# Optimization experiments

Measured on AMD Instinct MI355X. Metric: run time of the kernel, lower is better.

Reference implementation:

```python
import jax, jax.numpy as jnp
import numpy as np

B, D_IN, D, D_OUT, N_BLOCKS = 32768, 100, 1024, 1, 5
H = 0.1
EPS = 1e-4


def setup_inputs() -> dict:
    key = jax.random.key(0)
    ks = jax.random.split(key, 10)
    x = jax.random.normal(ks[0], (B, D_IN), dtype=jnp.float32)
    # first linear: D_IN -> D
    W0 = jax.random.normal(ks[1], (D, D_IN), dtype=jnp.float32) / np.sqrt(D_IN)
    b0 = jnp.zeros((D,), dtype=jnp.float32)
    # middle residual linears: D -> D, stacked over blocks
    Ws = jax.random.normal(ks[2], (N_BLOCKS, D, D), dtype=jnp.float32) / np.sqrt(D)
    bs = jnp.zeros((N_BLOCKS, D), dtype=jnp.float32)
    # brownian Linear(D, 1, bias=False) weight vectors, one per block
    bw = jax.random.normal(ks[3], (N_BLOCKS, D), dtype=jnp.float32) / np.sqrt(D)
    # last linear: D -> D_OUT
    Wlast = jax.random.normal(ks[4], (D_OUT, D), dtype=jnp.float32) / np.sqrt(D)
    blast = jnp.zeros((D_OUT,), dtype=jnp.float32)
    # torch.rand_like(out): uniform [0,1) noise per block
    noise = jax.random.uniform(ks[5], (N_BLOCKS, B, D), dtype=jnp.float32)
    return {"x": x, "W0": W0, "b0": b0, "Ws": Ws, "bs": bs,
            "bw": bw, "Wlast": Wlast, "blast": blast, "noise": noise}


def reference(x, W0, b0, Ws, bs, bw, Wlast, blast, noise):
    sqrt_h = H ** 0.5
    out = jnp.tanh(x @ W0.T + b0)  # [B, D]
    for i in range(N_BLOCKS):
        z = noise[i]  # [B, D]
        w = bw[i]     # [D]
        # product(): z @ (w w^T + eps I)^T = (z.w) w + eps z  (rank-1, O(D))
        proj = (z @ w)[:, None] * w + EPS * z
        out = out + H * jnp.tanh(out @ Ws[i].T + bs[i]) + sqrt_h * proj
    return out @ Wlast.T + blast  # [B, D_OUT]
```

## Files before the change

### kernel.cpp

```cpp
#include <hip/hip_runtime.h>
#include <hip/hip_bf16.h>


typedef unsigned short u16;
typedef __attribute__((ext_vector_type(8))) short short8;
typedef __attribute__((ext_vector_type(8))) u16 u16x8;
typedef __attribute__((ext_vector_type(4))) u16 u16x4;
typedef __attribute__((ext_vector_type(4))) float f32x4;
typedef __attribute__((ext_vector_type(16))) float f32x16;

#define BROWS 32768
#define DDIM 1024
#define NBLK 5
#define H_STEP 0.1f
#define SQRT_H 0.31622776601683794f

#define FENCE() asm volatile("" ::: "memory")
#define BARRIER() do { FENCE(); __builtin_amdgcn_s_barrier(); FENCE(); } while (0)

__device__ __forceinline__ float bf2f(u16 u) {
    return __uint_as_float(((unsigned)u) << 16);
}
__device__ __forceinline__ u16 f2bf(float f) {
    unsigned u = __float_as_uint(f);
    unsigned r = 0x7fffu + ((u >> 16) & 1u);
    return (u16)((u + r) >> 16);
}
__device__ __forceinline__ float fast_tanh(float s) {
    float e = __expf(2.0f * s);
    return 1.0f - 2.0f * __builtin_amdgcn_rcpf(e + 1.0f);
}

#define GLOAD_LDS16(g, l)                                                        \
    __builtin_amdgcn_global_load_lds(                                            \
        (const __attribute__((address_space(1))) unsigned int*)(const void*)(g), \
        (__attribute__((address_space(3))) unsigned int*)(void*)(l), 16, 0, 0)

__global__ __launch_bounds__(256) void pad_cvt(const float* __restrict__ src,
                                               u16* __restrict__ dst,
                                               int R, int C, int Cp) {
    int idx = blockIdx.x * 256 + threadIdx.x;
    if (idx >= R * Cp) return;
    int r = idx / Cp;
    int c = idx - r * Cp;
    float v = (c < C) ? src[(size_t)r * C + c] : 0.0f;
    dst[idx] = f2bf(v);
}

__global__ __launch_bounds__(256) void zw_kernel(const float* __restrict__ noise,
                                                 const float* __restrict__ bw,
                                                 float* __restrict__ zw) {
    int gw = (blockIdx.x * 256 + threadIdx.x) >> 6;
    int lane = threadIdx.x & 63;
    if (gw >= NBLK * BROWS) return;
    int i = gw >> 15;
    const float* zr = noise + (size_t)gw * DDIM;
    const float* wr = bw + i * DDIM;
    float s = 0.0f;
#pragma unroll
    for (int it = 0; it < 4; ++it) {
        int k = it * 256 + lane * 4;
        f32x4 z = *(const f32x4*)(zr + k);
        f32x4 w = *(const f32x4*)(wr + k);
        s += z.x * w.x + z.y * w.y + z.z * w.z + z.w * w.w;
    }
#pragma unroll
    for (int off = 32; off > 0; off >>= 1) s += __shfl_down(s, off, 64);
    if (lane == 0) zw[gw] = s;
}

template <int KK, int EPI>
__global__ __launch_bounds__(512, 2) void gemm256(const u16* __restrict__ Ag,
                                                  const u16* __restrict__ Bg,
                                                  const float* __restrict__ bias,
                                                  u16* __restrict__ outW,
                                                  const u16* __restrict__ outR,
                                                  const float* __restrict__ zw,
                                                  const float* __restrict__ bwv) {
    constexpr int NT = KK / 64;
    static_assert(NT >= 2 && (NT & 1) == 0, "NT even, >=2");
    __shared__ __align__(16) u16 smem[65536];
    char* lds = (char*)smem;

    const int bid = blockIdx.x;
    const int swz = (bid & 7) * 64 + (bid >> 3);
    const int row0 = (swz >> 2) * 256;
    const int col0 = (swz & 3) * 256;

    const int tid = threadIdx.x;
    const int lane = tid & 63;
    const int wid = tid >> 6;
    const int wm = wid >> 2;
    const int wn = wid & 3;

    const int lr = lane & 31;
    const int lk = (lane >> 5) * 8;
    const u16* aBase = Ag + (size_t)(row0 + lr) * KK + lk;
    const u16* bBase = Bg + (size_t)(col0 + lr) * KK + lk;

    auto stageQ = [&](int t, int kh, int j) {
        const int q = j * 8 + wid;
        const int isB = q >> 4;
        const int qq = q & 15;
        const int Mn = qq >> 1;
        const int ks = kh * 2 + (qq & 1);
        const u16* g = (isB ? bBase : aBase) + (size_t)Mn * 32 * KK + t * 64 + ks * 16;
        char* dst = lds + ((t & 1) << 16) + (isB << 15) + (Mn * 4 + ks) * 1024;
        GLOAD_LDS16(g, dst);
    };

    const int l16 = lane * 16;
    const int aA0 = l16 + (wm << 14);
    const int aA1 = aA0 + 65536;
    const int bA0 = l16 + 32768 + (wn << 13);
    const int bA1 = bA0 + 65536;

    f32x16 acc[4][2];
#pragma unroll
    for (int mt = 0; mt < 4; ++mt)
#pragma unroll
        for (int nt = 0; nt < 2; ++nt)
#pragma unroll
            for (int e = 0; e < 16; ++e) acc[mt][nt][e] = 0.f;

#define RDA(bufc, imm) (*(const short8*)(lds + ((bufc) ? aA1 : aA0) + (imm)))
#define RDB(bufc, imm) (*(const short8*)(lds + ((bufc) ? bA1 : bA0) + (imm)))
#define PHASE32(kh, bufc, STGS, VMW)                                                  \
    do {                                                                              \
        STGS;                                                                         \
        VMW;                                                                          \
        FENCE(); __builtin_amdgcn_s_barrier(); FENCE();                               \
        __builtin_amdgcn_s_setprio(1);                                                \
        short8 a0k0 = RDA(bufc, (0 * 4 + (kh) * 2 + 0) * 1024);                       \
        short8 a1k0 = RDA(bufc, (1 * 4 + (kh) * 2 + 0) * 1024);                       \
        short8 a2k0 = RDA(bufc, (2 * 4 + (kh) * 2 + 0) * 1024);                       \
        short8 a3k0 = RDA(bufc, (3 * 4 + (kh) * 2 + 0) * 1024);                       \
        short8 b0k0 = RDB(bufc, (0 * 4 + (kh) * 2 + 0) * 1024);                       \
        short8 b1k0 = RDB(bufc, (1 * 4 + (kh) * 2 + 0) * 1024);                       \
        short8 a0k1 = RDA(bufc, (0 * 4 + (kh) * 2 + 1) * 1024);                       \
        short8 a1k1 = RDA(bufc, (1 * 4 + (kh) * 2 + 1) * 1024);                       \
        short8 a2k1 = RDA(bufc, (2 * 4 + (kh) * 2 + 1) * 1024);                       \
        short8 a3k1 = RDA(bufc, (3 * 4 + (kh) * 2 + 1) * 1024);                       \
        short8 b0k1 = RDB(bufc, (0 * 4 + (kh) * 2 + 1) * 1024);                       \
        short8 b1k1 = RDB(bufc, (1 * 4 + (kh) * 2 + 1) * 1024);                       \
        acc[0][0] = __builtin_amdgcn_mfma_f32_32x32x16_bf16(a0k0, b0k0, acc[0][0], 0, 0, 0); \
        acc[0][1] = __builtin_amdgcn_mfma_f32_32x32x16_bf16(a0k0, b1k0, acc[0][1], 0, 0, 0); \
        acc[1][0] = __builtin_amdgcn_mfma_f32_32x32x16_bf16(a1k0, b0k0, acc[1][0], 0, 0, 0); \
        acc[1][1] = __builtin_amdgcn_mfma_f32_32x32x16_bf16(a1k0, b1k0, acc[1][1], 0, 0, 0); \
        acc[2][0] = __builtin_amdgcn_mfma_f32_32x32x16_bf16(a2k0, b0k0, acc[2][0], 0, 0, 0); \
        acc[2][1] = __builtin_amdgcn_mfma_f32_32x32x16_bf16(a2k0, b1k0, acc[2][1], 0, 0, 0); \
        acc[3][0] = __builtin_amdgcn_mfma_f32_32x32x16_bf16(a3k0, b0k0, acc[3][0], 0, 0, 0); \
        acc[3][1] = __builtin_amdgcn_mfma_f32_32x32x16_bf16(a3k0, b1k0, acc[3][1], 0, 0, 0); \
        acc[0][0] = __builtin_amdgcn_mfma_f32_32x32x16_bf16(a0k1, b0k1, acc[0][0], 0, 0, 0); \
        acc[0][1] = __builtin_amdgcn_mfma_f32_32x32x16_bf16(a0k1, b1k1, acc[0][1], 0, 0, 0); \
        acc[1][0] = __builtin_amdgcn_mfma_f32_32x32x16_bf16(a1k1, b0k1, acc[1][0], 0, 0, 0); \
        acc[1][1] = __builtin_amdgcn_mfma_f32_32x32x16_bf16(a1k1, b1k1, acc[1][1], 0, 0, 0); \
        acc[2][0] = __builtin_amdgcn_mfma_f32_32x32x16_bf16(a2k1, b0k1, acc[2][0], 0, 0, 0); \
        acc[2][1] = __builtin_amdgcn_mfma_f32_32x32x16_bf16(a2k1, b1k1, acc[2][1], 0, 0, 0); \
        acc[3][0] = __builtin_amdgcn_mfma_f32_32x32x16_bf16(a3k1, b0k1, acc[3][0], 0, 0, 0); \
        acc[3][1] = __builtin_amdgcn_mfma_f32_32x32x16_bf16(a3k1, b1k1, acc[3][1], 0, 0, 0); \
        __builtin_amdgcn_s_setprio(0);                                                \
        FENCE(); __builtin_amdgcn_s_barrier(); FENCE();                               \
    } while (0)
#define STG4(t, kh) do { stageQ(t, kh, 0); stageQ(t, kh, 1); stageQ(t, kh, 2); stageQ(t, kh, 3); } while (0)
#define VM4 asm volatile("s_waitcnt vmcnt(4)" ::: "memory")
#define VM0 asm volatile("s_waitcnt vmcnt(0)" ::: "memory")
#define NOSTG ((void)0)
#define NOVM ((void)0)

#define TILE32(t, c)                                                                  \
    do {                                                                              \
        PHASE32(0, c, STG4((t) + 1, 1), NOVM);                                        \
        PHASE32(1, c, STG4((t) + 2, 0), VM4);                                         \
    } while (0)

    STG4(0, 0); STG4(0, 1);
    STG4(1, 0);
    asm volatile("s_waitcnt vmcnt(4)" ::: "memory");
    BARRIER();

    for (int t2 = 0; t2 < NT / 2 - 1; ++t2) {
        TILE32(2 * t2, 0);
        TILE32(2 * t2 + 1, 1);
    }
    PHASE32(0, 0, STG4(NT - 1, 1), NOVM);
    PHASE32(1, 0, NOSTG, VM0);
    PHASE32(0, 1, NOSTG, NOVM);
    PHASE32(1, 1, NOSTG, NOVM);

    float bcol[2], bwc[2];
#pragma unroll
    for (int nt = 0; nt < 2; ++nt) {
        int cg = col0 + wn * 64 + nt * 32 + (lane & 31);
        bcol[nt] = bias[cg];
        if constexpr (EPI == 1) bwc[nt] = bwv[cg];
    }
    (void)bwc;

    char* wbase = lds + wid * 16384;
    const int cb = lane & 31;
    const int rq = (lane >> 5) * 4;
#pragma unroll
    for (int mt = 0; mt < 4; ++mt) {
#pragma unroll
        for (int nt = 0; nt < 2; ++nt) {
#pragma unroll
            for (int reg = 0; reg < 16; ++reg) {
                int lrow = mt * 32 + (reg & 3) + 8 * (reg >> 2) + rq;
                int lcol = nt * 32 + cb;
                float t = fast_tanh(acc[mt][nt][reg] + bcol[nt]);
                float d = (EPI == 0) ? t : H_STEP * t;
                int chunk = (lcol >> 3) ^ ((lrow >> 2) & 7);
                *(u16*)(wbase + lrow * 128 + (chunk << 4) + (lcol & 7) * 2) = f2bf(d);
            }
        }
    }

    const int gr_base = row0 + wm * 128;
    const int gc_base = col0 + wn * 64;
#pragma unroll
    for (int it = 0; it < 16; ++it) {
        int lrow = it * 8 + (lane >> 3);
        int chunk = lane & 7;
        int schunk = chunk ^ ((lrow >> 2) & 7);
        u16x8 d8 = *(const u16x8*)(wbase + lrow * 128 + (schunk << 4));
        int grow = gr_base + lrow;
        int gcol = gc_base + chunk * 8;
        size_t gidx = (size_t)grow * DDIM + gcol;
        u16x8 o8;
        if constexpr (EPI == 0) {
            o8 = d8;
        } else {
            u16x8 old8 = *(const u16x8*)(outR + gidx);
            float zr = SQRT_H * zw[grow];
            f32x4 bw0 = *(const f32x4*)(bwv + gcol);
            f32x4 bw1 = *(const f32x4*)(bwv + gcol + 4);
#pragma unroll
            for (int e = 0; e < 8; ++e) {
                float bwe = (e < 4) ? bw0[e] : bw1[e - 4];
                float v = bf2f(old8[e]) + bf2f(d8[e]) + zr * bwe;
                o8[e] = f2bf(v);
            }
        }
        *(u16x8*)(outW + gidx) = o8;
    }
#undef RDA
#undef RDB
#undef PHASE32
#undef STG4
#undef VM4
#undef VM0
#undef NOSTG
#undef NOVM
#undef TILE32
}

__global__ __launch_bounds__(256) void last_k(const u16* __restrict__ out,
                                              const float* __restrict__ wlast,
                                              const float* __restrict__ blast,
                                              float* __restrict__ y) {
    int gw = (blockIdx.x * 256 + threadIdx.x) >> 6;
    int lane = threadIdx.x & 63;
    if (gw >= BROWS) return;
    const u16* orow = out + (size_t)gw * DDIM;
    float s = 0.0f;
#pragma unroll
    for (int it = 0; it < 4; ++it) {
        int k = it * 256 + lane * 4;
        u16x4 o = *(const u16x4*)(orow + k);
        f32x4 w = *(const f32x4*)(wlast + k);
        s += bf2f(o.x) * w.x + bf2f(o.y) * w.y + bf2f(o.z) * w.z + bf2f(o.w) * w.w;
    }
#pragma unroll
    for (int off = 32; off > 0; off >>= 1) s += __shfl_down(s, off, 64);
    if (lane == 0) y[gw] = s + blast[0];
}

extern "C" void kernel_launch(void* const* d_in, const int* in_sizes, int n_in,
                              void* d_out, int out_size, void* d_ws, size_t ws_size,
                              hipStream_t stream) {
    const float* x     = (const float*)d_in[0];
    const float* W0    = (const float*)d_in[1];
    const float* b0    = (const float*)d_in[2];
    const float* Ws    = (const float*)d_in[3];
    const float* bs    = (const float*)d_in[4];
    const float* bw    = (const float*)d_in[5];
    const float* Wlast = (const float*)d_in[6];
    const float* blast = (const float*)d_in[7];
    const float* noise = (const float*)d_in[8];
    float* y = (float*)d_out;
    (void)in_sizes; (void)n_in; (void)out_size; (void)ws_size;

    char* ws = (char*)d_ws;
    size_t off = 0;
    auto alloc = [&](size_t bytes) {
        char* p = ws + off;
        off += (bytes + 255) & ~(size_t)255;
        return p;
    };
    u16* outB0 = (u16*)alloc((size_t)BROWS * DDIM * 2);
    u16* outB1 = (u16*)alloc((size_t)BROWS * DDIM * 2);
    u16* xb    = (u16*)alloc((size_t)BROWS * 128 * 2);
    u16* W0b   = (u16*)alloc((size_t)DDIM * 128 * 2);
    u16* Wsb   = (u16*)alloc((size_t)NBLK * DDIM * DDIM * 2);
    float* zw  = (float*)alloc((size_t)NBLK * BROWS * 4);

    pad_cvt<<<(BROWS * 128 + 255) / 256, 256, 0, stream>>>(x, xb, BROWS, 100, 128);
    pad_cvt<<<(DDIM * 128 + 255) / 256, 256, 0, stream>>>(W0, W0b, DDIM, 100, 128);
    pad_cvt<<<(NBLK * DDIM * DDIM + 255) / 256, 256, 0, stream>>>(Ws, Wsb, NBLK * DDIM, DDIM, DDIM);

    zw_kernel<<<(NBLK * BROWS) / 4, 256, 0, stream>>>(noise, bw, zw);

    gemm256<128, 0><<<512, 512, 0, stream>>>(xb, W0b, b0, outB0,
                                             nullptr, nullptr, nullptr);

    u16* cur = outB0;
    u16* nxt = outB1;
    for (int i = 0; i < NBLK; ++i) {
        gemm256<1024, 1><<<512, 512, 0, stream>>>(
            cur, Wsb + (size_t)i * DDIM * DDIM, bs + (size_t)i * DDIM, nxt, cur,
            zw + (size_t)i * BROWS, bw + (size_t)i * DDIM);
        u16* t = cur; cur = nxt; nxt = t;
    }

    last_k<<<BROWS / 4, 256, 0, stream>>>(cur, Wlast, blast, y);
}
```

Baseline: 666.8 us.

## Software-pipeline LDS fragment loads one k-step ahead of MFMAs in GEMM mainloop

Measured after the change: 673.4 us. Within noise of the previous version (+1.0%).

```diff
diff --git a/kernel.cpp b/kernel.cpp
--- a/kernel.cpp
+++ b/kernel.cpp
@@ -98,15 +98,16 @@
     const u16* aBase = Ag + (size_t)(row0 + lr) * KK + lk;
     const u16* bBase = Bg + (size_t)(col0 + lr) * KK + lk;
 
-    auto stageQ = [&](int t, int kh, int j) {
-        const int q = j * 8 + wid;
-        const int isB = q >> 4;
-        const int qq = q & 15;
-        const int Mn = qq >> 1;
-        const int ks = kh * 2 + (qq & 1);
-        const u16* g = (isB ? bBase : aBase) + (size_t)Mn * 32 * KK + t * 64 + ks * 16;
-        char* dst = lds + ((t & 1) << 16) + (isB << 15) + (Mn * 4 + ks) * 1024;
-        GLOAD_LDS16(g, dst);
+    auto stageU = [&](int t, int kh, int isB) {
+#pragma unroll
+        for (int j = 0; j < 2; ++j) {
+            const int idx = j * 8 + wid;
+            const int M = idx >> 1;
+            const int ks = kh * 2 + (idx & 1);
+            const u16* g = (isB ? bBase : aBase) + (size_t)M * 32 * KK + t * 64 + ks * 16;
+            char* dst = lds + ((t & 1) << 16) + (isB << 15) + (M * 4 + ks) * 1024;
+            GLOAD_LDS16(g, dst);
+        }
     };
 
     const int l16 = lane * 16;
@@ -115,6 +116,7 @@
     const int bA0 = l16 + 32768 + (wn << 13);
     const int bA1 = bA0 + 65536;
 
+    short8 afA[4], bfA[2], afB[4], bfB[2];
     f32x16 acc[4][2];
 #pragma unroll
     for (int mt = 0; mt < 4; ++mt)
@@ -125,77 +127,78 @@
 
 #define RDA(bufc, imm) (*(const short8*)(lds + ((bufc) ? aA1 : aA0) + (imm)))
 #define RDB(bufc, imm) (*(const short8*)(lds + ((bufc) ? bA1 : bA0) + (imm)))
-#define PHASE32(kh, bufc, STGS, VMW)                                                  \
-    do {                                                                              \
-        STGS;                                                                         \
+#define PF(afX, bfX, bufc, ks)                                                        \
+    do {                                                                              \
+        afX[0] = RDA(bufc, (0 * 4 + (ks)) * 1024);                                    \
+        afX[1] = RDA(bufc, (1 * 4 + (ks)) * 1024);                                    \
+        afX[2] = RDA(bufc, (2 * 4 + (ks)) * 1024);                                    \
+        afX[3] = RDA(bufc, (3 * 4 + (ks)) * 1024);                                    \
+        bfX[0] = RDB(bufc, (0 * 4 + (ks)) * 1024);                                    \
+        bfX[1] = RDB(bufc, (1 * 4 + (ks)) * 1024);                                    \
+    } while (0)
+#define MFMA8(af, bf)                                                                 \
+    do {                                                                              \
+        acc[0][0] = __builtin_amdgcn_mfma_f32_32x32x16_bf16(af[0], bf[0], acc[0][0], 0, 0, 0); \
+        acc[0][1] = __builtin_amdgcn_mfma_f32_32x32x16_bf16(af[0], bf[1], acc[0][1], 0, 0, 0); \
+        acc[1][0] = __builtin_amdgcn_mfma_f32_32x32x16_bf16(af[1], bf[0], acc[1][0], 0, 0, 0); \
+        acc[1][1] = __builtin_amdgcn_mfma_f32_32x32x16_bf16(af[1], bf[1], acc[1][1], 0, 0, 0); \
+        acc[2][0] = __builtin_amdgcn_mfma_f32_32x32x16_bf16(af[2], bf[0], acc[2][0], 0, 0, 0); \
+        acc[2][1] = __builtin_amdgcn_mfma_f32_32x32x16_bf16(af[2], bf[1], acc[2][1], 0, 0, 0); \
+        acc[3][0] = __builtin_amdgcn_mfma_f32_32x32x16_bf16(af[3], bf[0], acc[3][0], 0, 0, 0); \
+        acc[3][1] = __builtin_amdgcn_mfma_f32_32x32x16_bf16(af[3], bf[1], acc[3][1], 0, 0, 0); \
+    } while (0)
+#define VM4 asm volatile("s_waitcnt vmcnt(4)" ::: "memory")
+#define VM0 asm volatile("s_waitcnt vmcnt(0)" ::: "memory")
+#define NOVM ((void)0)
+#define NOSTG ((void)0)
+#define PH(afC, bfC, afN, bfN, bufN, ksN, VMW, STG)                                   \
+    do {                                                                              \
         VMW;                                                                          \
-        FENCE(); __builtin_amdgcn_s_barrier(); FENCE();                               \
+        PF(afN, bfN, bufN, ksN);                                                      \
+        STG;                                                                          \
         __builtin_amdgcn_s_setprio(1);                                                \
-        short8 a0k0 = RDA(bufc, (0 * 4 + (kh) * 2 + 0) * 1024);                       \
-        short8 a1k0 = RDA(bufc, (1 * 4 + (kh) * 2 + 0) * 1024);                       \
-        short8 a2k0 = RDA(bufc, (2 * 4 + (kh) * 2 + 0) * 1024);                       \
-        short8 a3k0 = RDA(bufc, (3 * 4 + (kh) * 2 + 0) * 1024);                       \
-        short8 b0k0 = RDB(bufc, (0 * 4 + (kh) * 2 + 0) * 1024);                       \
-        short8 b1k0 = RDB(bufc, (1 * 4 + (kh) * 2 + 0) * 1024);                       \
-        short8 a0k1 = RDA(bufc, (0 * 4 + (kh) * 2 + 1) * 1024);                       \
-        short8 a1k1 = RDA(bufc, (1 * 4 + (kh) * 2 + 1) * 1024);                       \
-        short8 a2k1 = RDA(bufc, (2 * 4 + (kh) * 2 + 1) * 1024);                       \
-        short8 a3k1 = RDA(bufc, (3 * 4 + (kh) * 2 + 1) * 1024);                       \
-        short8 b0k1 = RDB(bufc, (0 * 4 + (kh) * 2 + 1) * 1024);                       \
-        short8 b1k1 = RDB(bufc, (1 * 4 + (kh) * 2 + 1) * 1024);                       \
-        acc[0][0] = __builtin_amdgcn_mfma_f32_32x32x16_bf16(a0k0, b0k0, acc[0][0], 0, 0, 0); \
-        acc[0][1] = __builtin_amdgcn_mfma_f32_32x32x16_bf16(a0k0, b1k0, acc[0][1], 0, 0, 0); \
-        acc[1][0] = __builtin_amdgcn_mfma_f32_32x32x16_bf16(a1k0, b0k0, acc[1][0], 0, 0, 0); \
-        acc[1][1] = __builtin_amdgcn_mfma_f32_32x32x16_bf16(a1k0, b1k0, acc[1][1], 0, 0, 0); \
-        acc[2][0] = __builtin_amdgcn_mfma_f32_32x32x16_bf16(a2k0, b0k0, acc[2][0], 0, 0, 0); \
-        acc[2][1] = __builtin_amdgcn_mfma_f32_32x32x16_bf16(a2k0, b1k0, acc[2][1], 0, 0, 0); \
-        acc[3][0] = __builtin_amdgcn_mfma_f32_32x32x16_bf16(a3k0, b0k0, acc[3][0], 0, 0, 0); \
-        acc[3][1] = __builtin_amdgcn_mfma_f32_32x32x16_bf16(a3k0, b1k0, acc[3][1], 0, 0, 0); \
-        acc[0][0] = __builtin_amdgcn_mfma_f32_32x32x16_bf16(a0k1, b0k1, acc[0][0], 0, 0, 0); \
-        acc[0][1] = __builtin_amdgcn_mfma_f32_32x32x16_bf16(a0k1, b1k1, acc[0][1], 0, 0, 0); \
-        acc[1][0] = __builtin_amdgcn_mfma_f32_32x32x16_bf16(a1k1, b0k1, acc[1][0], 0, 0, 0); \
-        acc[1][1] = __builtin_amdgcn_mfma_f32_32x32x16_bf16(a1k1, b1k1, acc[1][1], 0, 0, 0); \
-        acc[2][0] = __builtin_amdgcn_mfma_f32_32x32x16_bf16(a2k1, b0k1, acc[2][0], 0, 0, 0); \
-        acc[2][1] = __builtin_amdgcn_mfma_f32_32x32x16_bf16(a2k1, b1k1, acc[2][1], 0, 0, 0); \
-        acc[3][0] = __builtin_amdgcn_mfma_f32_32x32x16_bf16(a3k1, b0k1, acc[3][0], 0, 0, 0); \
-        acc[3][1] = __builtin_amdgcn_mfma_f32_32x32x16_bf16(a3k1, b1k1, acc[3][1], 0, 0, 0); \
+        MFMA8(afC, bfC);                                                              \
         __builtin_amdgcn_s_setprio(0);                                                \
         FENCE(); __builtin_amdgcn_s_barrier(); FENCE();                               \
     } while (0)
-#define STG4(t, kh) do { stageQ(t, kh, 0); stageQ(t, kh, 1); stageQ(t, kh, 2); stageQ(t, kh, 3); } while (0)
-#define VM4 asm volatile("s_waitcnt vmcnt(4)" ::: "memory")
-#define VM0 asm volatile("s_waitcnt vmcnt(0)" ::: "memory")
-#define NOSTG ((void)0)
-#define NOVM ((void)0)
-
-#define TILE32(t, c)                                                                  \
-    do {                                                                              \
-        PHASE32(0, c, STG4((t) + 1, 1), NOVM);                                        \
-        PHASE32(1, c, STG4((t) + 2, 0), VM4);                                         \
-    } while (0)
-
-    STG4(0, 0); STG4(0, 1);
-    STG4(1, 0);
+#define PH_LAST(afC, bfC)                                                             \
+    do {                                                                              \
+        __builtin_amdgcn_s_setprio(1);                                                \
+        MFMA8(afC, bfC);                                                              \
+        __builtin_amdgcn_s_setprio(0);                                                \
+        FENCE(); __builtin_amdgcn_s_barrier(); FENCE();                               \
+    } while (0)
+
+#define TILE(t, c)                                                                    \
+    do {                                                                              \
+        PH(afA, bfA, afB, bfB, c, 1, VM4, stageU((t) + 1, 1, 0));                     \
+        PH(afB, bfB, afA, bfA, c, 2, VM4, stageU((t) + 1, 1, 1));                     \
+        PH(afA, bfA, afB, bfB, c, 3, VM4, stageU((t) + 2, 0, 0));                     \
+        PH(afB, bfB, afA, bfA, (c) ^ 1, 0, VM4, stageU((t) + 2, 0, 1));               \
+    } while (0)
+
+    stageU(0, 0, 0); stageU(0, 0, 1); stageU(0, 1, 0); stageU(0, 1, 1);
+    stageU(1, 0, 0); stageU(1, 0, 1);
     asm volatile("s_waitcnt vmcnt(4)" ::: "memory");
     BARRIER();
+    PF(afA, bfA, 0, 0);
 
     for (int t2 = 0; t2 < NT / 2 - 1; ++t2) {
-        TILE32(2 * t2, 0);
-        TILE32(2 * t2 + 1, 1);
-    }
-    PHASE32(0, 0, STG4(NT - 1, 1), NOVM);
-    PHASE32(1, 0, NOSTG, VM0);
-    PHASE32(0, 1, NOSTG, NOVM);
-    PHASE32(1, 1, NOSTG, NOVM);
-
-    float bcol[2], bwc[2];
-#pragma unroll
-    for (int nt = 0; nt < 2; ++nt) {
-        int cg = col0 + wn * 64 + nt * 32 + (lane & 31);
-        bcol[nt] = bias[cg];
-        if constexpr (EPI == 1) bwc[nt] = bwv[cg];
-    }
-    (void)bwc;
+        TILE(2 * t2, 0);
+        TILE(2 * t2 + 1, 1);
+    }
+    PH(afA, bfA, afB, bfB, 0, 1, VM4, stageU(NT - 1, 1, 0));
+    PH(afB, bfB, afA, bfA, 0, 2, VM4, stageU(NT - 1, 1, 1));
+    PH(afA, bfA, afB, bfB, 0, 3, VM4, NOSTG);
+    PH(afB, bfB, afA, bfA, 1, 0, VM4, NOSTG);
+    PH(afA, bfA, afB, bfB, 1, 1, VM0, NOSTG);
+    PH(afB, bfB, afA, bfA, 1, 2, NOVM, NOSTG);
+    PH(afA, bfA, afB, bfB, 1, 3, NOVM, NOSTG);
+    PH_LAST(afB, bfB);
+
+    float bcol[2];
+#pragma unroll
+    for (int nt = 0; nt < 2; ++nt) bcol[nt] = bias[col0 + wn * 64 + nt * 32 + (lane & 31)];
 
     char* wbase = lds + wid * 16384;
     const int cb = lane & 31;
@@ -246,13 +249,15 @@
     }
 #undef RDA
 #undef RDB
-#undef PHASE32
-#undef STG4
+#undef PF
+#undef MFMA8
 #undef VM4
 #undef VM0
+#undef NOVM
 #undef NOSTG
-#undef NOVM
-#undef TILE32
+#undef PH
+#undef PH_LAST
+#undef TILE
 }
 
 __global__ __launch_bounds__(256) void last_k(const u16* __restrict__ out,
```
